# Kernel tuning notes

Measured on AMD Instinct MI355X. Metric: run time of the kernel, lower is better.

## Reference

```python
import jax, jax.numpy as jnp
import numpy as np

CHANNELS = 256   # input_channels == output_channels == res_feature channels
HIDDEN = 128
NODES = 7

def setup_inputs() -> dict:
    key = jax.random.key(0)
    k1, k2, k3, k4, k5 = jax.random.split(key, 5)
    batch, d, h, w = 2, 16, 64, 64
    inp = jax.random.normal(k1, (1, batch, NODES, HIDDEN), dtype=jnp.float32)
    res_feature = jax.random.normal(k2, (batch, CHANNELS, d, h, w), dtype=jnp.float32)
    # xavier_uniform-style init
    def xavier(k, shape):
        fan_in, fan_out = shape[0], shape[1]
        a = jnp.sqrt(6.0 / (fan_in + fan_out))
        return jax.random.uniform(k, shape, dtype=jnp.float32, minval=-a, maxval=a)
    node_fea_for_res = xavier(k3, (CHANNELS, NODES))
    node_fea_for_hidden = xavier(k4, (HIDDEN, 1))
    weight = xavier(k5, (HIDDEN, CHANNELS))
    return {"inp": inp, "res_feature": res_feature,
            "node_fea_for_res": node_fea_for_res,
            "node_fea_for_hidden": node_fea_for_hidden,
            "weight": weight}

def reference(inp, res_feature, node_fea_for_res, node_fea_for_hidden, weight):
    b, c, d, h, w = res_feature.shape
    # [b, dhw, c]
    rf = res_feature.reshape(b, c, d * h * w).transpose(0, 2, 1)
    # scores from residual features: [b, dhw, nodes]
    n1 = rf @ node_fea_for_res
    # scores from node hidden features (constant over spatial dim): [b, nodes]
    # (original expands input over dhw then matmuls with [hidden,1]; equivalent)
    n2 = (inp[0] @ node_fea_for_hidden)[..., 0]
    attn = jax.nn.softmax(n1 + n2[:, None, :], axis=-1)  # [b, dhw, nodes]
    new_weight = inp[0] @ weight                          # [b, nodes, c]
    feature_out = jnp.einsum('bpn,bnc->bpc', attn, new_weight)  # [b, dhw, c]
    feature_out = feature_out.transpose(0, 2, 1).reshape(b, c, d, h, w)
    return jax.nn.relu(feature_out)
```

## Files before the change

kernel.cpp:

```cpp
#include <hip/hip_runtime.h>

#define DHW    65536
#define NCH    256
#define NNODE  7
#define NHID   128
#define NBATCH 2

typedef float vf4 __attribute__((ext_vector_type(4)));

__device__ inline float4 f4fma(float4 v, float w, float4 a) {
    a.x = fmaf(v.x, w, a.x); a.y = fmaf(v.y, w, a.y);
    a.z = fmaf(v.z, w, a.z); a.w = fmaf(v.w, w, a.w);
    return a;
}

__global__ void prep_kernel(const float* __restrict__ inp,
                            const float* __restrict__ nfh,
                            const float* __restrict__ weight,
                            const float* __restrict__ w1,
                            float* __restrict__ nwt,
                            float* __restrict__ n2g,
                            float* __restrict__ w1p)
{
    const int bn = blockIdx.x;
    const int b  = bn / NNODE;
    const int n  = bn % NNODE;
    const int t  = threadIdx.x;
    const float* ih = inp + (b * NNODE + n) * NHID;

    float acc = 0.f;
    #pragma unroll 8
    for (int h = 0; h < NHID; ++h)
        acc = fmaf(ih[h], weight[h * NCH + t], acc);
    nwt[(b * NCH + t) * 8 + n] = acc;

    if (bn == 0) {
        #pragma unroll
        for (int k = 0; k < NNODE; ++k) w1p[t * 8 + k] = w1[t * NNODE + k];
        w1p[t * 8 + 7] = 0.f;
    }

    __shared__ float red[NHID];
    if (t < NHID) red[t] = ih[t] * nfh[t];
    __syncthreads();
    for (int s = NHID / 2; s > 0; s >>= 1) {
        if (t < s) red[t] += red[t + s];
        __syncthreads();
    }
    if (t == 0) n2g[b * 8 + n] = red[0];
}

__global__ __launch_bounds__(256, 2)
void main_kernel(const float* __restrict__ rf,
                 const float* __restrict__ w1p,
                 const float* __restrict__ nwt,
                 const float* __restrict__ n2g,
                 float* __restrict__ out)
{
    __shared__ float4 red[NNODE][4][64];

    const int t    = threadIdx.x;
    const int lane = t & 63;
    const int wv   = __builtin_amdgcn_readfirstlane(t >> 6);
    const int blk  = blockIdx.x;
    const int b    = blk >> 8;
    const int i4   = ((blk & 255) << 6) + lane;
    const int c0   = wv << 6;

    const vf4* rp = (const vf4*)rf + (((size_t)(b * NCH + c0)) << 14) + i4;
    const float4* wq = (const float4*)w1p + (c0 << 1);

    float4 a0 = {0,0,0,0}, a1 = {0,0,0,0}, a2 = {0,0,0,0}, a3 = {0,0,0,0};
    float4 a4 = {0,0,0,0}, a5 = {0,0,0,0}, a6 = {0,0,0,0};

    #pragma unroll 8
    for (int ci = 0; ci < 64; ++ci) {
        vf4 vv = __builtin_nontemporal_load(&rp[(size_t)ci << 14]);
        float4 v = make_float4(vv.x, vv.y, vv.z, vv.w);
        float4 wa = wq[ci * 2];
        float4 wb = wq[ci * 2 + 1];
        a0 = f4fma(v, wa.x, a0);
        a1 = f4fma(v, wa.y, a1);
        a2 = f4fma(v, wa.z, a2);
        a3 = f4fma(v, wa.w, a3);
        a4 = f4fma(v, wb.x, a4);
        a5 = f4fma(v, wb.y, a5);
        a6 = f4fma(v, wb.z, a6);
    }

    red[0][wv][lane] = a0;  red[1][wv][lane] = a1;  red[2][wv][lane] = a2;
    red[3][wv][lane] = a3;  red[4][wv][lane] = a4;  red[5][wv][lane] = a5;
    red[6][wv][lane] = a6;
    __syncthreads();

    const float* n2 = n2g + b * 8;
    float4 s[NNODE];
    #pragma unroll
    for (int n = 0; n < NNODE; ++n) {
        float4 r = red[n][0][lane];
        #pragma unroll
        for (int w = 1; w < 4; ++w) {
            float4 q = red[n][w][lane];
            r.x += q.x; r.y += q.y; r.z += q.z; r.w += q.w;
        }
        r.x += n2[n]; r.y += n2[n]; r.z += n2[n]; r.w += n2[n];
        s[n] = r;
    }
    float4 m = s[0];
    #pragma unroll
    for (int n = 1; n < NNODE; ++n) {
        m.x = fmaxf(m.x, s[n].x); m.y = fmaxf(m.y, s[n].y);
        m.z = fmaxf(m.z, s[n].z); m.w = fmaxf(m.w, s[n].w);
    }
    float4 sum = {0,0,0,0};
    float4 e[NNODE];
    #pragma unroll
    for (int n = 0; n < NNODE; ++n) {
        e[n].x = __expf(s[n].x - m.x); e[n].y = __expf(s[n].y - m.y);
        e[n].z = __expf(s[n].z - m.z); e[n].w = __expf(s[n].w - m.w);
        sum.x += e[n].x; sum.y += e[n].y; sum.z += e[n].z; sum.w += e[n].w;
    }
    float4 inv = make_float4(1.f/sum.x, 1.f/sum.y, 1.f/sum.z, 1.f/sum.w);
    #pragma unroll
    for (int n = 0; n < NNODE; ++n) {
        e[n].x *= inv.x; e[n].y *= inv.y; e[n].z *= inv.z; e[n].w *= inv.w;
    }

    const float4* nq = (const float4*)nwt + ((b * NCH + c0) << 1);
    vf4* op = (vf4*)out + (((size_t)(b * NCH + c0)) << 14) + i4;
    #pragma unroll 8
    for (int ci = 0; ci < 64; ++ci) {
        float4 na = nq[ci * 2];
        float4 nb = nq[ci * 2 + 1];
        float4 o = {0,0,0,0};
        o = f4fma(e[0], na.x, o);
        o = f4fma(e[1], na.y, o);
        o = f4fma(e[2], na.z, o);
        o = f4fma(e[3], na.w, o);
        o = f4fma(e[4], nb.x, o);
        o = f4fma(e[5], nb.y, o);
        o = f4fma(e[6], nb.z, o);
        vf4 ov;
        ov.x = fmaxf(o.x, 0.f); ov.y = fmaxf(o.y, 0.f);
        ov.z = fmaxf(o.z, 0.f); ov.w = fmaxf(o.w, 0.f);
        __builtin_nontemporal_store(ov, &op[(size_t)ci << 14]);
    }
}

extern "C" void kernel_launch(void* const* d_in, const int* in_sizes, int n_in,
                              void* d_out, int out_size, void* d_ws, size_t ws_size,
                              hipStream_t stream) {
    const float* inp = (const float*)d_in[0];
    const float* rf  = (const float*)d_in[1];
    const float* w1  = (const float*)d_in[2];
    const float* nfh = (const float*)d_in[3];
    const float* wgt = (const float*)d_in[4];
    float* out = (float*)d_out;

    float* nwt = (float*)d_ws;
    float* n2g = nwt + NBATCH * NCH * 8;
    float* w1p = n2g + NBATCH * 8;

    prep_kernel<<<NBATCH * NNODE, 256, 0, stream>>>(inp, nfh, wgt, w1, nwt, n2g, w1p);
    main_kernel<<<NBATCH * 256, 256, 0, stream>>>(rf, w1p, nwt, n2g, out);
}
```

Measured before the change: 242.7 us.

## Split fused attention/output kernel into separate attn and output kernels

Splits the main kernel into an attention kernel that computes softmax weights into a workspace buffer and a second kernel that reads those weights and writes the 256-channel output with twice as many blocks. Only one wave per block now does the softmax, removing redundant softmax work in the other three waves. The output stage gets more blocks and higher occupancy for the write-heavy phase. The cost is an extra launch plus a write and reread of the attention tensor through memory.

Result: no change. 244.4 us (+0.7%).

```diff
diff --git a/kernel.cpp b/kernel.cpp
--- a/kernel.cpp
+++ b/kernel.cpp
@@ -51,11 +51,10 @@
 }
 
 __global__ __launch_bounds__(256, 2)
-void main_kernel(const float* __restrict__ rf,
+void attn_kernel(const float* __restrict__ rf,
                  const float* __restrict__ w1p,
-                 const float* __restrict__ nwt,
                  const float* __restrict__ n2g,
-                 float* __restrict__ out)
+                 float* __restrict__ attn)
 {
     __shared__ float4 red[NNODE][4][64];
 
@@ -93,6 +92,8 @@
     red[6][wv][lane] = a6;
     __syncthreads();
 
+    if (wv != 0) return;
+
     const float* n2 = n2g + b * 8;
     float4 s[NNODE];
     #pragma unroll
@@ -121,15 +122,40 @@
         sum.x += e[n].x; sum.y += e[n].y; sum.z += e[n].z; sum.w += e[n].w;
     }
     float4 inv = make_float4(1.f/sum.x, 1.f/sum.y, 1.f/sum.z, 1.f/sum.w);
+    float4* ap = (float4*)attn;
     #pragma unroll
     for (int n = 0; n < NNODE; ++n) {
-        e[n].x *= inv.x; e[n].y *= inv.y; e[n].z *= inv.z; e[n].w *= inv.w;
+        float4 o;
+        o.x = e[n].x * inv.x; o.y = e[n].y * inv.y;
+        o.z = e[n].z * inv.z; o.w = e[n].w * inv.w;
+        ap[((n * NBATCH + b) << 14) + i4] = o;
     }
+}
+
+__global__ __launch_bounds__(256, 4)
+void out_kernel(const float* __restrict__ attn,
+                const float* __restrict__ nwt,
+                float* __restrict__ out)
+{
+    const int t    = threadIdx.x;
+    const int lane = t & 63;
+    const int wv   = __builtin_amdgcn_readfirstlane(t >> 6);
+    const int blk  = blockIdx.x;
+    const int b    = blk >> 9;
+    const int half = (blk >> 8) & 1;
+    const int i4   = ((blk & 255) << 6) + lane;
+    const int c0   = (half << 7) + (wv << 5);
+
+    const float4* ap = (const float4*)attn;
+    float4 e[NNODE];
+    #pragma unroll
+    for (int n = 0; n < NNODE; ++n)
+        e[n] = ap[((n * NBATCH + b) << 14) + i4];
 
     const float4* nq = (const float4*)nwt + ((b * NCH + c0) << 1);
     vf4* op = (vf4*)out + (((size_t)(b * NCH + c0)) << 14) + i4;
     #pragma unroll 8
-    for (int ci = 0; ci < 64; ++ci) {
+    for (int ci = 0; ci < 32; ++ci) {
         float4 na = nq[ci * 2];
         float4 nb = nq[ci * 2 + 1];
         float4 o = {0,0,0,0};
@@ -157,10 +183,12 @@
     const float* wgt = (const float*)d_in[4];
     float* out = (float*)d_out;
 
-    float* nwt = (float*)d_ws;
-    float* n2g = nwt + NBATCH * NCH * 8;
-    float* w1p = n2g + NBATCH * 8;
+    float* nwt  = (float*)d_ws;
+    float* n2g  = nwt + NBATCH * NCH * 8;
+    float* w1p  = n2g + NBATCH * 8;
+    float* attn = w1p + NCH * 8;
 
     prep_kernel<<<NBATCH * NNODE, 256, 0, stream>>>(inp, nfh, wgt, w1, nwt, n2g, w1p);
-    main_kernel<<<NBATCH * 256, 256, 0, stream>>>(rf, w1p, nwt, n2g, out);
+    attn_kernel<<<NBATCH * 256, 256, 0, stream>>>(rf, w1p, n2g, attn);
+    out_kernel<<<NBATCH * 512, 256, 0, stream>>>(attn, nwt, out);
 }
```

## Fuse prep kernel into main kernel, recomputing node weights per block

Applied to the files above, without the earlier changes.

Removes the separate prep launch: each block now computes its slice of the node-weight projection (inp @ weight), the per-node hidden score via wave shuffles, and reads the unpadded w1 directly. This drops one kernel launch and the workspace round-trip, at the cost of redundant per-block recomputation (128-step loop over weight with 7 accumulators) before the memory-bound streaming loop. The extra shared memory for node weights may also affect occupancy.

After: 248.3 us. 2.3% more time.

```diff
diff --git a/kernel.cpp b/kernel.cpp
--- a/kernel.cpp
+++ b/kernel.cpp
@@ -14,50 +14,16 @@
     return a;
 }
 
-__global__ void prep_kernel(const float* __restrict__ inp,
-                            const float* __restrict__ nfh,
-                            const float* __restrict__ weight,
-                            const float* __restrict__ w1,
-                            float* __restrict__ nwt,
-                            float* __restrict__ n2g,
-                            float* __restrict__ w1p)
-{
-    const int bn = blockIdx.x;
-    const int b  = bn / NNODE;
-    const int n  = bn % NNODE;
-    const int t  = threadIdx.x;
-    const float* ih = inp + (b * NNODE + n) * NHID;
-
-    float acc = 0.f;
-    #pragma unroll 8
-    for (int h = 0; h < NHID; ++h)
-        acc = fmaf(ih[h], weight[h * NCH + t], acc);
-    nwt[(b * NCH + t) * 8 + n] = acc;
-
-    if (bn == 0) {
-        #pragma unroll
-        for (int k = 0; k < NNODE; ++k) w1p[t * 8 + k] = w1[t * NNODE + k];
-        w1p[t * 8 + 7] = 0.f;
-    }
-
-    __shared__ float red[NHID];
-    if (t < NHID) red[t] = ih[t] * nfh[t];
-    __syncthreads();
-    for (int s = NHID / 2; s > 0; s >>= 1) {
-        if (t < s) red[t] += red[t + s];
-        __syncthreads();
-    }
-    if (t == 0) n2g[b * 8 + n] = red[0];
-}
-
 __global__ __launch_bounds__(256, 2)
-void main_kernel(const float* __restrict__ rf,
-                 const float* __restrict__ w1p,
-                 const float* __restrict__ nwt,
-                 const float* __restrict__ n2g,
-                 float* __restrict__ out)
+void fused_kernel(const float* __restrict__ rf,
+                  const float* __restrict__ inp,
+                  const float* __restrict__ w1g,
+                  const float* __restrict__ nfh,
+                  const float* __restrict__ weight,
+                  float* __restrict__ out)
 {
     __shared__ float4 red[NNODE][4][64];
+    __shared__ float4 nwt4[4][64][2];
 
     const int t    = threadIdx.x;
     const int lane = t & 63;
@@ -66,9 +32,41 @@
     const int b    = blk >> 8;
     const int i4   = ((blk & 255) << 6) + lane;
     const int c0   = wv << 6;
+    const int c    = c0 + lane;
+
+    const float* ib = inp + b * NNODE * NHID;
+
+    float nv0 = 0.f, nv1 = 0.f, nv2 = 0.f, nv3 = 0.f;
+    float nv4 = 0.f, nv5 = 0.f, nv6 = 0.f;
+    #pragma unroll 4
+    for (int h = 0; h < NHID; ++h) {
+        float wgt = weight[h * NCH + c];
+        nv0 = fmaf(ib[0 * NHID + h], wgt, nv0);
+        nv1 = fmaf(ib[1 * NHID + h], wgt, nv1);
+        nv2 = fmaf(ib[2 * NHID + h], wgt, nv2);
+        nv3 = fmaf(ib[3 * NHID + h], wgt, nv3);
+        nv4 = fmaf(ib[4 * NHID + h], wgt, nv4);
+        nv5 = fmaf(ib[5 * NHID + h], wgt, nv5);
+        nv6 = fmaf(ib[6 * NHID + h], wgt, nv6);
+    }
+    nwt4[wv][lane][0] = make_float4(nv0, nv1, nv2, nv3);
+    nwt4[wv][lane][1] = make_float4(nv4, nv5, nv6, 0.f);
+
+    float p[NNODE];
+    {
+        const float nf0 = nfh[lane], nf1 = nfh[lane + 64];
+        #pragma unroll
+        for (int n = 0; n < NNODE; ++n)
+            p[n] = ib[n * NHID + lane] * nf0 + ib[n * NHID + lane + 64] * nf1;
+        #pragma unroll
+        for (int s = 32; s > 0; s >>= 1) {
+            #pragma unroll
+            for (int n = 0; n < NNODE; ++n)
+                p[n] += __shfl_xor(p[n], s, 64);
+        }
+    }
 
     const vf4* rp = (const vf4*)rf + (((size_t)(b * NCH + c0)) << 14) + i4;
-    const float4* wq = (const float4*)w1p + (c0 << 1);
 
     float4 a0 = {0,0,0,0}, a1 = {0,0,0,0}, a2 = {0,0,0,0}, a3 = {0,0,0,0};
     float4 a4 = {0,0,0,0}, a5 = {0,0,0,0}, a6 = {0,0,0,0};
@@ -77,15 +75,14 @@
     for (int ci = 0; ci < 64; ++ci) {
         vf4 vv = __builtin_nontemporal_load(&rp[(size_t)ci << 14]);
         float4 v = make_float4(vv.x, vv.y, vv.z, vv.w);
-        float4 wa = wq[ci * 2];
-        float4 wb = wq[ci * 2 + 1];
-        a0 = f4fma(v, wa.x, a0);
-        a1 = f4fma(v, wa.y, a1);
-        a2 = f4fma(v, wa.z, a2);
-        a3 = f4fma(v, wa.w, a3);
-        a4 = f4fma(v, wb.x, a4);
-        a5 = f4fma(v, wb.y, a5);
-        a6 = f4fma(v, wb.z, a6);
+        const float* wr = w1g + (c0 + ci) * NNODE;
+        a0 = f4fma(v, wr[0], a0);
+        a1 = f4fma(v, wr[1], a1);
+        a2 = f4fma(v, wr[2], a2);
+        a3 = f4fma(v, wr[3], a3);
+        a4 = f4fma(v, wr[4], a4);
+        a5 = f4fma(v, wr[5], a5);
+        a6 = f4fma(v, wr[6], a6);
     }
 
     red[0][wv][lane] = a0;  red[1][wv][lane] = a1;  red[2][wv][lane] = a2;
@@ -93,7 +90,6 @@
     red[6][wv][lane] = a6;
     __syncthreads();
 
-    const float* n2 = n2g + b * 8;
     float4 s[NNODE];
     #pragma unroll
     for (int n = 0; n < NNODE; ++n) {
@@ -103,7 +99,7 @@
             float4 q = red[n][w][lane];
             r.x += q.x; r.y += q.y; r.z += q.z; r.w += q.w;
         }
-        r.x += n2[n]; r.y += n2[n]; r.z += n2[n]; r.w += n2[n];
+        r.x += p[n]; r.y += p[n]; r.z += p[n]; r.w += p[n];
         s[n] = r;
     }
     float4 m = s[0];
@@ -126,12 +122,11 @@
         e[n].x *= inv.x; e[n].y *= inv.y; e[n].z *= inv.z; e[n].w *= inv.w;
     }
 
-    const float4* nq = (const float4*)nwt + ((b * NCH + c0) << 1);
     vf4* op = (vf4*)out + (((size_t)(b * NCH + c0)) << 14) + i4;
     #pragma unroll 8
     for (int ci = 0; ci < 64; ++ci) {
-        float4 na = nq[ci * 2];
-        float4 nb = nq[ci * 2 + 1];
+        float4 na = nwt4[wv][ci][0];
+        float4 nb = nwt4[wv][ci][1];
         float4 o = {0,0,0,0};
         o = f4fma(e[0], na.x, o);
         o = f4fma(e[1], na.y, o);
@@ -157,10 +152,7 @@
     const float* wgt = (const float*)d_in[4];
     float* out = (float*)d_out;
 
-    float* nwt = (float*)d_ws;
-    float* n2g = nwt + NBATCH * NCH * 8;
-    float* w1p = n2g + NBATCH * 8;
+    (void)d_ws; (void)ws_size;
 
-    prep_kernel<<<NBATCH * NNODE, 256, 0, stream>>>(inp, nfh, wgt, w1, nwt, n2g, w1p);
-    main_kernel<<<NBATCH * 256, 256, 0, stream>>>(rf, w1p, nwt, n2g, out);
+    fused_kernel<<<NBATCH * 256, 256, 0, stream>>>(rf, inp, w1, nfh, wgt, out);
 }
```

## Split spatial tiles across wave halves with shuffle reduction and LDS-staged weights

Applied to the files above, without the earlier changes.

Each block now covers 32 float4 spatial columns instead of 64, and the two halves of every wave take alternating channels. This doubles the grid to 1024 blocks and halves the per-thread channel loop. Partial scores are combined across wave halves with xor-shuffles before the LDS reduction. The projection and output weights are staged into shared memory, and occupancy is raised to 3 blocks per SIMD. The aim is more blocks and more memory parallelism for this bandwidth-bound kernel, at the cost of extra shuffles, an extra barrier and more LDS per block.

Measured after the change: 242.5 us. About the same (-0.1%).

```diff
diff --git a/kernel.cpp b/kernel.cpp
--- a/kernel.cpp
+++ b/kernel.cpp
@@ -50,35 +50,50 @@
     if (t == 0) n2g[b * 8 + n] = red[0];
 }
 
-__global__ __launch_bounds__(256, 2)
+__global__ __launch_bounds__(256, 3)
 void main_kernel(const float* __restrict__ rf,
                  const float* __restrict__ w1p,
                  const float* __restrict__ nwt,
                  const float* __restrict__ n2g,
                  float* __restrict__ out)
 {
-    __shared__ float4 red[NNODE][4][64];
+    __shared__ float4 w1l[512];
+    __shared__ float4 nwl[512];
+    __shared__ float4 red[NNODE][4][32];
 
     const int t    = threadIdx.x;
     const int lane = t & 63;
     const int wv   = __builtin_amdgcn_readfirstlane(t >> 6);
     const int blk  = blockIdx.x;
-    const int b    = blk >> 8;
-    const int i4   = ((blk & 255) << 6) + lane;
-    const int c0   = wv << 6;
-
-    const vf4* rp = (const vf4*)rf + (((size_t)(b * NCH + c0)) << 14) + i4;
-    const float4* wq = (const float4*)w1p + (c0 << 1);
+    const int b    = blk >> 9;
+    const int g    = blk & 511;
+    const int col  = lane & 31;
+    const int half = lane >> 5;
+    const int c0   = (wv << 6) + half;
+    const int base4 = (g << 5) + col;
+
+    {
+        const float4* wsrc = (const float4*)w1p;
+        const float4* nsrc = (const float4*)(nwt + b * NCH * 8);
+        w1l[t]       = wsrc[t];
+        w1l[t + 256] = wsrc[t + 256];
+        nwl[t]       = nsrc[t];
+        nwl[t + 256] = nsrc[t + 256];
+    }
+    __syncthreads();
+
+    const vf4* rp = (const vf4*)rf + (((size_t)(b * NCH + c0)) << 14) + base4;
 
     float4 a0 = {0,0,0,0}, a1 = {0,0,0,0}, a2 = {0,0,0,0}, a3 = {0,0,0,0};
     float4 a4 = {0,0,0,0}, a5 = {0,0,0,0}, a6 = {0,0,0,0};
 
     #pragma unroll 8
-    for (int ci = 0; ci < 64; ++ci) {
-        vf4 vv = __builtin_nontemporal_load(&rp[(size_t)ci << 14]);
+    for (int ci = 0; ci < 32; ++ci) {
+        vf4 vv = __builtin_nontemporal_load(&rp[(size_t)(ci * 2) << 14]);
         float4 v = make_float4(vv.x, vv.y, vv.z, vv.w);
-        float4 wa = wq[ci * 2];
-        float4 wb = wq[ci * 2 + 1];
+        const int c = c0 + ci * 2;
+        float4 wa = w1l[c * 2];
+        float4 wb = w1l[c * 2 + 1];
         a0 = f4fma(v, wa.x, a0);
         a1 = f4fma(v, wa.y, a1);
         a2 = f4fma(v, wa.z, a2);
@@ -88,19 +103,38 @@
         a6 = f4fma(v, wb.z, a6);
     }
 
-    red[0][wv][lane] = a0;  red[1][wv][lane] = a1;  red[2][wv][lane] = a2;
-    red[3][wv][lane] = a3;  red[4][wv][lane] = a4;  red[5][wv][lane] = a5;
-    red[6][wv][lane] = a6;
+    #pragma unroll
+    for (int k = 0; k < 1; ++k) { }
+    a0.x += __shfl_xor(a0.x, 32); a0.y += __shfl_xor(a0.y, 32);
+    a0.z += __shfl_xor(a0.z, 32); a0.w += __shfl_xor(a0.w, 32);
+    a1.x += __shfl_xor(a1.x, 32); a1.y += __shfl_xor(a1.y, 32);
+    a1.z += __shfl_xor(a1.z, 32); a1.w += __shfl_xor(a1.w, 32);
+    a2.x += __shfl_xor(a2.x, 32); a2.y += __shfl_xor(a2.y, 32);
+    a2.z += __shfl_xor(a2.z, 32); a2.w += __shfl_xor(a2.w, 32);
+    a3.x += __shfl_xor(a3.x, 32); a3.y += __shfl_xor(a3.y, 32);
+    a3.z += __shfl_xor(a3.z, 32); a3.w += __shfl_xor(a3.w, 32);
+    a4.x += __shfl_xor(a4.x, 32); a4.y += __shfl_xor(a4.y, 32);
+    a4.z += __shfl_xor(a4.z, 32); a4.w += __shfl_xor(a4.w, 32);
+    a5.x += __shfl_xor(a5.x, 32); a5.y += __shfl_xor(a5.y, 32);
+    a5.z += __shfl_xor(a5.z, 32); a5.w += __shfl_xor(a5.w, 32);
+    a6.x += __shfl_xor(a6.x, 32); a6.y += __shfl_xor(a6.y, 32);
+    a6.z += __shfl_xor(a6.z, 32); a6.w += __shfl_xor(a6.w, 32);
+
+    if (half == 0) {
+        red[0][wv][col] = a0;  red[1][wv][col] = a1;  red[2][wv][col] = a2;
+        red[3][wv][col] = a3;  red[4][wv][col] = a4;  red[5][wv][col] = a5;
+        red[6][wv][col] = a6;
+    }
     __syncthreads();
 
     const float* n2 = n2g + b * 8;
     float4 s[NNODE];
     #pragma unroll
     for (int n = 0; n < NNODE; ++n) {
-        float4 r = red[n][0][lane];
+        float4 r = red[n][0][col];
         #pragma unroll
         for (int w = 1; w < 4; ++w) {
-            float4 q = red[n][w][lane];
+            float4 q = red[n][w][col];
             r.x += q.x; r.y += q.y; r.z += q.z; r.w += q.w;
         }
         r.x += n2[n]; r.y += n2[n]; r.z += n2[n]; r.w += n2[n];
@@ -126,12 +160,12 @@
         e[n].x *= inv.x; e[n].y *= inv.y; e[n].z *= inv.z; e[n].w *= inv.w;
     }
 
-    const float4* nq = (const float4*)nwt + ((b * NCH + c0) << 1);
-    vf4* op = (vf4*)out + (((size_t)(b * NCH + c0)) << 14) + i4;
+    vf4* op = (vf4*)out + (((size_t)(b * NCH + c0)) << 14) + base4;
     #pragma unroll 8
-    for (int ci = 0; ci < 64; ++ci) {
-        float4 na = nq[ci * 2];
-        float4 nb = nq[ci * 2 + 1];
+    for (int ci = 0; ci < 32; ++ci) {
+        const int c = c0 + ci * 2;
+        float4 na = nwl[c * 2];
+        float4 nb = nwl[c * 2 + 1];
         float4 o = {0,0,0,0};
         o = f4fma(e[0], na.x, o);
         o = f4fma(e[1], na.y, o);
@@ -143,7 +177,7 @@
         vf4 ov;
         ov.x = fmaxf(o.x, 0.f); ov.y = fmaxf(o.y, 0.f);
         ov.z = fmaxf(o.z, 0.f); ov.w = fmaxf(o.w, 0.f);
-        __builtin_nontemporal_store(ov, &op[(size_t)ci << 14]);
+        __builtin_nontemporal_store(ov, &op[(size_t)(ci * 2) << 14]);
     }
 }
 
@@ -162,5 +196,5 @@
     float* w1p = n2g + NBATCH * 8;
 
     prep_kernel<<<NBATCH * NNODE, 256, 0, stream>>>(inp, nfh, wgt, w1, nwt, n2g, w1p);
-    main_kernel<<<NBATCH * 256, 256, 0, stream>>>(rf, w1p, nwt, n2g, out);
-}
+    main_kernel<<<NBATCH * 512, 256, 0, stream>>>(rf, w1p, nwt, n2g, out);
+}
```
